# Kernel tuning notes

Measured on AMD Instinct MI355X. Metric: run time of the kernel, lower is better.

## Reference

```python
import jax, jax.numpy as jnp
import numpy as np

N_EMBD = 1024
N_HEAD = 16


def setup_inputs() -> dict:
    key = jax.random.key(0)
    ks = jax.random.split(key, 5)
    B, T, C = 2, 2048, N_EMBD
    x = jax.random.normal(ks[0], (B, T, C), dtype=jnp.float32)
    # parameters (stored as (in, out); forward uses x @ W + b, equivalent to torch Linear)
    s1 = 1.0 / np.sqrt(C)
    W_attn = jax.random.normal(ks[1], (C, 3 * C), dtype=jnp.float32) * s1
    b_attn = jnp.zeros((3 * C,), dtype=jnp.float32)
    W_proj = jax.random.normal(ks[2], (C, C), dtype=jnp.float32) * s1
    b_proj = jnp.zeros((C,), dtype=jnp.float32)
    return {"x": x, "W_attn": W_attn, "b_attn": b_attn, "W_proj": W_proj, "b_proj": b_proj}


def reference(x, W_attn, b_attn, W_proj, b_proj):
    B, T, C = x.shape
    H = N_HEAD
    D = C // H  # head dim
    qkv = x @ W_attn + b_attn                       # [B, T, 3C]
    q, k, v = jnp.split(qkv, 3, axis=-1)
    # [B, H, T, D]
    q = q.reshape(B, T, H, D).transpose(0, 2, 1, 3)
    k = k.reshape(B, T, H, D).transpose(0, 2, 1, 3)
    v = v.reshape(B, T, H, D).transpose(0, 2, 1, 3)
    scale = 1.0 / jnp.sqrt(jnp.asarray(D, dtype=q.dtype))
    wei = jnp.einsum("bhqd,bhkd->bhqk", q, k) * scale  # [B, H, T, T]
    causal = jnp.tril(jnp.ones((T, T), dtype=bool))
    wei = jnp.where(causal[None, None, :, :], wei, -jnp.inf)
    wei = jax.nn.softmax(wei, axis=-1)
    y = jnp.einsum("bhqk,bhkd->bhqd", wei, v)          # [B, H, T, D]
    y = y.transpose(0, 2, 1, 3).reshape(B, T, C)
    return y @ W_proj + b_proj
```

## Files before the change

### kernel.cpp

```cpp
#include <hip/hip_runtime.h>
#include <hip/hip_bf16.h>

typedef __attribute__((ext_vector_type(8))) short short8;
typedef __attribute__((ext_vector_type(4))) float floatx4;
#define BF16 __hip_bfloat16

__device__ __forceinline__ unsigned short f2bf(float f) {
  unsigned int u = __builtin_bit_cast(unsigned int, f);
  unsigned int r = (u + 0x7FFFu + ((u >> 16) & 1u)) >> 16;
  return (unsigned short)r;
}

__device__ __forceinline__ void gload_lds16(const void* g, void* l) {
  __builtin_amdgcn_global_load_lds(
      (const __attribute__((address_space(1))) unsigned int*)g,
      (__attribute__((address_space(3))) unsigned int*)l, 16, 0, 0);
}

__global__ __launch_bounds__(256)
void cvt_bf16(const float* __restrict__ in, unsigned short* __restrict__ out, int n) {
  int i = (blockIdx.x * 256 + threadIdx.x) * 8;
  if (i >= n) return;
  float4 a = *(const float4*)(in + i);
  float4 b = *(const float4*)(in + i + 4);
  short8 v;
  v[0] = (short)f2bf(a.x); v[1] = (short)f2bf(a.y);
  v[2] = (short)f2bf(a.z); v[3] = (short)f2bf(a.w);
  v[4] = (short)f2bf(b.x); v[5] = (short)f2bf(b.y);
  v[6] = (short)f2bf(b.z); v[7] = (short)f2bf(b.w);
  *(short8*)(out + i) = v;
}

__global__ __launch_bounds__(256)
void transpose_cvt(const float* __restrict__ in, unsigned short* __restrict__ out,
                   int K, int N) {
  __shared__ float tile[64][65];
  const int nb = N >> 6;
  const int tn = blockIdx.x % nb, tk = blockIdx.x / nb;
  const int n0 = tn << 6, k0 = tk << 6;
  const int tid = threadIdx.x;
#pragma unroll
  for (int c = 0; c < 4; ++c) {
    int t = tid + c * 256;
    int r = t >> 4, col = (t & 15) << 2;
    float4 v = *(const float4*)(in + (size_t)(k0 + r) * N + n0 + col);
    tile[r][col] = v.x; tile[r][col + 1] = v.y;
    tile[r][col + 2] = v.z; tile[r][col + 3] = v.w;
  }
  __syncthreads();
#pragma unroll
  for (int c = 0; c < 2; ++c) {
    int t = tid + c * 256;
    int r = t >> 3, col = (t & 7) << 3;
    short8 v;
#pragma unroll
    for (int j = 0; j < 8; ++j) v[j] = (short)f2bf(tile[col + j][r]);
    *(short8*)(out + (size_t)(n0 + r) * K + k0 + col) = v;
  }
}

template <int EPI>
__global__ __launch_bounds__(256, 2)
void gemm_bt(const BF16* __restrict__ A, const BF16* __restrict__ Bt,
             const float* __restrict__ bias, void* __restrict__ outv,
             int M, int N, int K) {
  const int tid = threadIdx.x;
  const int w = tid >> 6, l = tid & 63;
  const int lr = l & 15, lg = l >> 4;
  const int nbx = N >> 7;
  const int bm = blockIdx.x / nbx, bn = blockIdx.x % nbx;
  const int row0 = bm << 7, col0 = bn << 7;
  const int wr = (w >> 1) << 6, wc = (w & 1) << 6;

  __shared__ __align__(16) BF16 ldsA[128 * 32];
  __shared__ __align__(16) BF16 ldsB[128 * 32];

  floatx4 acc[4][4] = {};

  for (int k0 = 0; k0 < K; k0 += 32) {
#pragma unroll
    for (int c = 0; c < 2; ++c) {
      int t = w * 64 + l + c * 256;
      int ar = t >> 2, ac = (t & 3) << 3;
      gload_lds16(A + (size_t)(row0 + ar) * K + k0 + ac, ldsA + w * 512 + c * 2048);
      gload_lds16(Bt + (size_t)(col0 + ar) * K + k0 + ac, ldsB + w * 512 + c * 2048);
    }
    __syncthreads();
    short8 af[4], bf[4];
#pragma unroll
    for (int m = 0; m < 4; ++m)
      af[m] = *(const short8*)(ldsA + (wr + m * 16 + lr) * 32 + lg * 8);
#pragma unroll
    for (int n = 0; n < 4; ++n)
      bf[n] = *(const short8*)(ldsB + (wc + n * 16 + lr) * 32 + lg * 8);
#pragma unroll
    for (int m = 0; m < 4; ++m)
#pragma unroll
      for (int n = 0; n < 4; ++n)
        acc[m][n] = __builtin_amdgcn_mfma_f32_16x16x32_bf16(af[m], bf[n], acc[m][n], 0, 0, 0);
    __syncthreads();
  }

#pragma unroll
  for (int m = 0; m < 4; ++m)
#pragma unroll
    for (int n = 0; n < 4; ++n)
#pragma unroll
      for (int j = 0; j < 4; ++j) {
        int row = row0 + wr + m * 16 + lg * 4 + j;
        int col = col0 + wc + n * 16 + lr;
        float v = acc[m][n][j] + bias[col];
        if (EPI == 0) {
          BF16* out = (BF16*)outv;
          int s = col >> 10, cc = col & 1023;
          int hh = cc >> 6, dd = cc & 63;
          int bb = row >> 11, tt = row & 2047;
          size_t addr;
          if (s == 2)
            addr = (size_t)8388608 + (((size_t)bb * 16 + hh) * 64 + dd) * 2048 + tt;
          else
            addr = (size_t)s * 4194304 + (((size_t)bb * 16 + hh) * 2048 + tt) * 64 + dd;
          out[addr] = __float2bfloat16(v);
        } else {
          float* out = (float*)outv;
          out[(size_t)row * N + col] = v;
        }
      }
}

__global__ __launch_bounds__(256, 4)
void flash_attn(const BF16* __restrict__ qkv, BF16* __restrict__ y) {
  const int T = 2048;
  const int i = blockIdx.x;
  const int xcd = i & 7, s = i >> 3;
  const int qt = 31 - (s >> 2);
  const int bh = xcd * 4 + (s & 3);
  const int b = bh >> 4, h = bh & 15;
  const int q0 = qt << 6;
  const int tid = threadIdx.x, w = tid >> 6, l = tid & 63;
  const int lr = l & 15, lg = l >> 4;

  const BF16* Q  = qkv + (size_t)bh * T * 64;
  const BF16* Kp = qkv + 4194304 + (size_t)bh * T * 64;
  const BF16* Vt = qkv + 8388608 + (size_t)bh * 64 * T;

  __shared__ __align__(16) BF16 ldsK[2][4096];
  __shared__ __align__(16) BF16 ldsV[2][4096];
  __shared__ __align__(16) BF16 ldsP[4096];

  const float C1 = 0.18033688011112042f;
  const float C2 = 17.312340490667562f;
  const int swzl = (lr & 7) << 3;
  const int nt = qt + 1;

  short8 qf[2];
#pragma unroll
  for (int c = 0; c < 2; ++c)
    qf[c] = *(const short8*)(Q + (size_t)(q0 + w * 16 + lr) * 64 + c * 32 + lg * 8);

  floatx4 acc_o[4] = {};
  float lsum[4] = {0.f, 0.f, 0.f, 0.f};

#define STAGE(JT, BUF)                                                        \
  {                                                                           \
    const int j0_ = (JT) << 6;                                                \
    _Pragma("unroll")                                                         \
    for (int c = 0; c < 2; ++c) {                                             \
      int t = w * 64 + l + c * 256;                                           \
      int r = t >> 3;                                                         \
      int ch = (t & 7) ^ (r & 7);                                             \
      gload_lds16(Kp + (size_t)(j0_ + r) * 64 + ch * 8,                       \
                  &ldsK[BUF][w * 512 + c * 2048]);                            \
      gload_lds16(Vt + (size_t)r * T + j0_ + ch * 8,                          \
                  &ldsV[BUF][w * 512 + c * 2048]);                            \
    }                                                                         \
  }

  STAGE(0, 0);

  for (int jt = 0; jt < nt; ++jt) {
    const int j0 = jt << 6;
    const int cur = jt & 1;
    if (jt + 1 < nt) {
      STAGE(jt + 1, cur ^ 1);
      asm volatile("s_waitcnt vmcnt(4)" ::: "memory");
    } else {
      asm volatile("s_waitcnt vmcnt(0)" ::: "memory");
    }
    __builtin_amdgcn_s_barrier();

    floatx4 accs[4] = {};
    __builtin_amdgcn_s_setprio(1);
#pragma unroll
    for (int c = 0; c < 2; ++c)
#pragma unroll
      for (int n = 0; n < 4; ++n) {
        short8 kf = *(const short8*)(&ldsK[cur][(n * 16 + lr) * 64 + ((c * 32 + lg * 8) ^ swzl)]);
        accs[n] = __builtin_amdgcn_mfma_f32_16x16x32_bf16(qf[c], kf, accs[n], 0, 0, 0);
      }
    __builtin_amdgcn_s_setprio(0);

    const bool diag = (jt == qt);
#pragma unroll
    for (int n = 0; n < 4; ++n)
#pragma unroll
      for (int j = 0; j < 4; ++j) {
        float p = exp2f(fmaf(accs[n][j], C1, -C2));
        if (diag) {
          int key = j0 + n * 16 + lr;
          int qrow = q0 + w * 16 + lg * 4 + j;
          if (key > qrow) p = 0.f;
        }
        lsum[j] += p;
        int rowp = lg * 4 + j;
        ldsP[w * 1024 + rowp * 64 + ((n * 16 + lr) ^ ((rowp & 7) << 3))] = __float2bfloat16(p);
      }

    __builtin_amdgcn_s_setprio(1);
#pragma unroll
    for (int c = 0; c < 2; ++c) {
      short8 pf = *(const short8*)(ldsP + w * 1024 + lr * 64 + ((c * 32 + lg * 8) ^ swzl));
#pragma unroll
      for (int n = 0; n < 4; ++n) {
        short8 vf = *(const short8*)(&ldsV[cur][(n * 16 + lr) * 64 + ((c * 32 + lg * 8) ^ swzl)]);
        acc_o[n] = __builtin_amdgcn_mfma_f32_16x16x32_bf16(pf, vf, acc_o[n], 0, 0, 0);
      }
    }
    __builtin_amdgcn_s_setprio(0);
    __builtin_amdgcn_s_barrier();
  }
#undef STAGE

  float inv[4];
#pragma unroll
  for (int j = 0; j < 4; ++j) {
    float ssum = lsum[j];
    ssum += __shfl_xor(ssum, 1, 64);
    ssum += __shfl_xor(ssum, 2, 64);
    ssum += __shfl_xor(ssum, 4, 64);
    ssum += __shfl_xor(ssum, 8, 64);
    inv[j] = 1.0f / ssum;
  }
#pragma unroll
  for (int n = 0; n < 4; ++n)
#pragma unroll
    for (int j = 0; j < 4; ++j) {
      int qrow = q0 + w * 16 + lg * 4 + j;
      int dd = n * 16 + lr;
      y[((size_t)b * 2048 + qrow) * 1024 + h * 64 + dd] =
          __float2bfloat16(acc_o[n][j] * inv[j]);
    }
}

extern "C" void kernel_launch(void* const* d_in, const int* in_sizes, int n_in,
                              void* d_out, int out_size, void* d_ws, size_t ws_size,
                              hipStream_t stream) {
  const float* x      = (const float*)d_in[0];
  const float* W_attn = (const float*)d_in[1];
  const float* b_attn = (const float*)d_in[2];
  const float* W_proj = (const float*)d_in[3];
  const float* b_proj = (const float*)d_in[4];
  float* out = (float*)d_out;
  BF16* ws  = (BF16*)d_ws;

  BF16* xb      = ws;
  BF16* wt_attn = xb + 4194304;
  BF16* wt_proj = wt_attn + 3145728;
  BF16* qkv     = wt_proj + 1048576;
  BF16* y       = qkv + 12582912;

  hipLaunchKernelGGL(cvt_bf16, dim3(2048), dim3(256), 0, stream,
                     x, (unsigned short*)xb, 4194304);
  hipLaunchKernelGGL(transpose_cvt, dim3(48 * 16), dim3(256), 0, stream,
                     W_attn, (unsigned short*)wt_attn, 1024, 3072);
  hipLaunchKernelGGL(transpose_cvt, dim3(16 * 16), dim3(256), 0, stream,
                     W_proj, (unsigned short*)wt_proj, 1024, 1024);
  hipLaunchKernelGGL(gemm_bt<0>, dim3(32 * 24), dim3(256), 0, stream,
                     xb, wt_attn, b_attn, (void*)qkv, 4096, 3072, 1024);
  hipLaunchKernelGGL(flash_attn, dim3(1024), dim3(256), 0, stream, qkv, y);
  hipLaunchKernelGGL(gemm_bt<1>, dim3(32 * 8), dim3(256), 0, stream,
                     y, wt_proj, b_proj, (void*)out, 4096, 1024, 1024);
}
```

Baseline: 125.0 us.

## Keep attention probabilities in registers via transposed QK^T and permlane swaps

```diff
diff --git a/kernel.cpp b/kernel.cpp
--- a/kernel.cpp
+++ b/kernel.cpp
@@ -3,12 +3,19 @@
 
 typedef __attribute__((ext_vector_type(8))) short short8;
 typedef __attribute__((ext_vector_type(4))) float floatx4;
+typedef __attribute__((ext_vector_type(4))) unsigned int uintx4;
 #define BF16 __hip_bfloat16
 
 __device__ __forceinline__ unsigned short f2bf(float f) {
   unsigned int u = __builtin_bit_cast(unsigned int, f);
   unsigned int r = (u + 0x7FFFu + ((u >> 16) & 1u)) >> 16;
   return (unsigned short)r;
+}
+
+__device__ __forceinline__ unsigned int cvt_pk_bf16(float lo, float hi) {
+  unsigned int r;
+  asm("v_cvt_pk_bf16_f32 %0, %1, %2" : "=v"(r) : "v"(lo), "v"(hi));
+  return r;
 }
 
 __device__ __forceinline__ void gload_lds16(const void* g, void* l) {
@@ -133,8 +140,11 @@
   const int T = 2048;
   const int i = blockIdx.x;
   const int xcd = i & 7, s = i >> 3;
-  const int qt = 31 - (s >> 2);
-  const int bh = xcd * 4 + (s & 3);
+  const int par = (s ^ (s >> 5)) & 1;
+  const int rnk = ((s >> 5) << 4) | ((s & 31) >> 1);
+  const int bh = xcd * 4 + (rnk & 3);
+  const int hq = rnk >> 2;
+  const int qt = par ? hq : (31 - hq);
   const int b = bh >> 4, h = bh & 15;
   const int q0 = qt << 6;
   const int tid = threadIdx.x, w = tid >> 6, l = tid & 63;
@@ -145,8 +155,7 @@
   const BF16* Vt = qkv + 8388608 + (size_t)bh * 64 * T;
 
   __shared__ __align__(16) BF16 ldsK[2][4096];
-  __shared__ __align__(16) BF16 ldsV[2][4096];
-  __shared__ __align__(16) BF16 ldsP[4096];
+  __shared__ __align__(16) BF16 ldsV[2][6144];
 
   const float C1 = 0.18033688011112042f;
   const float C2 = 17.312340490667562f;
@@ -159,7 +168,7 @@
     qf[c] = *(const short8*)(Q + (size_t)(q0 + w * 16 + lr) * 64 + c * 32 + lg * 8);
 
   floatx4 acc_o[4] = {};
-  float lsum[4] = {0.f, 0.f, 0.f, 0.f};
+  float lsum = 0.f;
 
 #define STAGE(JT, BUF)                                                        \
   {                                                                           \
@@ -196,30 +205,36 @@
 #pragma unroll
       for (int n = 0; n < 4; ++n) {
         short8 kf = *(const short8*)(&ldsK[cur][(n * 16 + lr) * 64 + ((c * 32 + lg * 8) ^ swzl)]);
-        accs[n] = __builtin_amdgcn_mfma_f32_16x16x32_bf16(qf[c], kf, accs[n], 0, 0, 0);
+        accs[n] = __builtin_amdgcn_mfma_f32_16x16x32_bf16(kf, qf[c], accs[n], 0, 0, 0);
       }
     __builtin_amdgcn_s_setprio(0);
 
     const bool diag = (jt == qt);
+    const int qrow = q0 + w * 16 + lr;
 #pragma unroll
     for (int n = 0; n < 4; ++n)
 #pragma unroll
       for (int j = 0; j < 4; ++j) {
         float p = exp2f(fmaf(accs[n][j], C1, -C2));
-        if (diag) {
-          int key = j0 + n * 16 + lr;
-          int qrow = q0 + w * 16 + lg * 4 + j;
-          if (key > qrow) p = 0.f;
-        }
-        lsum[j] += p;
-        int rowp = lg * 4 + j;
-        ldsP[w * 1024 + rowp * 64 + ((n * 16 + lr) ^ ((rowp & 7) << 3))] = __float2bfloat16(p);
+        if (diag && (j0 + n * 16 + lg * 4 + j > qrow)) p = 0.f;
+        lsum += p;
+        accs[n][j] = p;
       }
 
     __builtin_amdgcn_s_setprio(1);
 #pragma unroll
     for (int c = 0; c < 2; ++c) {
-      short8 pf = *(const short8*)(ldsP + w * 1024 + lr * 64 + ((c * 32 + lg * 8) ^ swzl));
+      unsigned int a0 = cvt_pk_bf16(accs[2 * c][0], accs[2 * c][1]);
+      unsigned int b0 = cvt_pk_bf16(accs[2 * c + 1][0], accs[2 * c + 1][1]);
+      unsigned int a1 = cvt_pk_bf16(accs[2 * c][2], accs[2 * c][3]);
+      unsigned int b1 = cvt_pk_bf16(accs[2 * c + 1][2], accs[2 * c + 1][3]);
+      asm("v_permlane32_swap_b32 %0, %1" : "+v"(a0), "+v"(b0));
+      asm("v_permlane32_swap_b32 %0, %1" : "+v"(a1), "+v"(b1));
+      asm("v_permlane16_swap_b32 %0, %1" : "+v"(a0), "+v"(b0));
+      asm("v_permlane16_swap_b32 %0, %1" : "+v"(a1), "+v"(b1));
+      uintx4 pw;
+      pw[0] = a0; pw[1] = a1; pw[2] = b0; pw[3] = b1;
+      short8 pf = __builtin_bit_cast(short8, pw);
 #pragma unroll
       for (int n = 0; n < 4; ++n) {
         short8 vf = *(const short8*)(&ldsV[cur][(n * 16 + lr) * 64 + ((c * 32 + lg * 8) ^ swzl)]);
@@ -231,23 +246,19 @@
   }
 #undef STAGE
 
+  lsum += __shfl_xor(lsum, 16, 64);
+  lsum += __shfl_xor(lsum, 32, 64);
+  float inv_own = 1.0f / lsum;
   float inv[4];
 #pragma unroll
-  for (int j = 0; j < 4; ++j) {
-    float ssum = lsum[j];
-    ssum += __shfl_xor(ssum, 1, 64);
-    ssum += __shfl_xor(ssum, 2, 64);
-    ssum += __shfl_xor(ssum, 4, 64);
-    ssum += __shfl_xor(ssum, 8, 64);
-    inv[j] = 1.0f / ssum;
-  }
+  for (int j = 0; j < 4; ++j) inv[j] = __shfl(inv_own, lg * 4 + j, 64);
 #pragma unroll
   for (int n = 0; n < 4; ++n)
 #pragma unroll
     for (int j = 0; j < 4; ++j) {
-      int qrow = q0 + w * 16 + lg * 4 + j;
+      int qr = q0 + w * 16 + lg * 4 + j;
       int dd = n * 16 + lr;
-      y[((size_t)b * 2048 + qrow) * 1024 + h * 64 + dd] =
+      y[((size_t)b * 2048 + qr) * 1024 + h * 64 + dd] =
           __float2bfloat16(acc_o[n][j] * inv[j]);
     }
 }
```

After: 118.0 us. 5.6% less time.
